# Optimization experiments

Measured on AMD Instinct MI355X. Metric: run time of the kernel, lower is better.

Reference implementation:

```python
import jax, jax.numpy as jnp
import numpy as np

N_QUBITS = 12
N_LAYERS = 3
DIM = 2 ** N_QUBITS


def _ry(t):
    # RY(t) = [[cos(t/2), -sin(t/2)], [sin(t/2), cos(t/2)]]; t scalar or (B,)
    c, s = jnp.cos(t / 2), jnp.sin(t / 2)
    return jnp.stack([jnp.stack([c, -s], -1), jnp.stack([s, c], -1)], -2).astype(jnp.complex64)


def _rx(t):
    c = jnp.cos(t / 2).astype(jnp.complex64)
    s = (-1j) * jnp.sin(t / 2).astype(jnp.complex64)
    return jnp.stack([jnp.stack([c, s], -1), jnp.stack([s, c], -1)], -2)


def _rz(t):
    e = jnp.exp(-0.5j * t.astype(jnp.complex64))
    z = jnp.zeros_like(e)
    return jnp.stack([jnp.stack([e, z], -1), jnp.stack([z, jnp.conj(e)], -1)], -2)


def _apply_1q(state, U, wire):
    # state: (B, 2^n); U: (2,2) shared or (B,2,2) per-sample
    B = state.shape[0]
    L, R = 2 ** wire, 2 ** (N_QUBITS - wire - 1)
    s = state.reshape(B, L, 2, R)
    sub = 'ab' if U.ndim == 2 else 'xab'
    s = jnp.einsum(f'{sub},xlbr->xlar', U, s)
    return s.reshape(B, DIM)


def _apply_cnot(state, ctrl):
    # CNOT on adjacent wires (ctrl, ctrl+1): flip target where control=1
    B = state.shape[0]
    L, R = 2 ** ctrl, 2 ** (N_QUBITS - ctrl - 2)
    s = state.reshape(B, L, 2, 2, R)
    s = jnp.concatenate([s[:, :, :1], s[:, :, 1:, ::-1]], axis=2)
    return s.reshape(B, DIM)


def _circuit(x, params):
    B = x.shape[0]
    state = jnp.zeros((B, DIM), jnp.complex64).at[:, 0].set(1.0)
    # input encoding: RY(x_i) on wire i (per-sample angles)
    for i in range(N_QUBITS):
        state = _apply_1q(state, _ry(x[:, i]), i)
    for layer in range(N_LAYERS):
        for q in range(N_QUBITS):
            state = _apply_1q(state, _ry(params[layer, q, 0]), q)
            state = _apply_1q(state, _rx(params[layer, q, 1]), q)
            state = _apply_1q(state, _rz(params[layer, q, 2]), q)
        for q in range(N_QUBITS - 1):
            state = _apply_cnot(state, q)
    probs = jnp.abs(state) ** 2  # wire 0 is the MSB, matching qml.probs
    p2 = probs[:, :2]
    return p2 / jnp.sum(p2, axis=1, keepdims=True)


def setup_inputs() -> dict:
    key = jax.random.key(0)
    k1, k2 = jax.random.split(key)
    x = (jax.random.uniform(k1, (8192, N_QUBITS), jnp.float32) * 2.0 - 1.0) * jnp.pi
    params = jax.random.normal(k2, (N_LAYERS, N_QUBITS, 3), jnp.float32) * 0.1
    return {"x": x, "params": params}


def reference(x, params):
    return _circuit(x, params)
```

## Files before the change

kernel.cpp:

```cpp
#include <hip/hip_runtime.h>
#include <math.h>

#define NQ  12
#define DIM 4096


__device__ float M_dev[DIM * 4];

struct Gate { float g00r, g00i, g01r, g01i; };

__device__ __forceinline__ Gate make_gate(const float* __restrict__ params,
                                          int layer, int q) {
  float p0 = params[(layer*NQ + q)*3 + 0];
  float p1 = params[(layer*NQ + q)*3 + 1];
  float p2 = params[(layer*NQ + q)*3 + 2];
  float s0, c0, s1, c1, sz, cz;
  __sincosf(0.5f*p0, &s0, &c0);
  __sincosf(0.5f*p1, &s1, &c1);
  __sincosf(0.5f*p2, &sz, &cz);
  float ur = c0*c1, ui = s0*s1, wr = s0*c1, wi = c0*s1;
  Gate g;
  g.g00r = cz*ur - sz*ui;  g.g00i = cz*ui + sz*ur;
  g.g01r = cz*wr + sz*wi;  g.g01i = cz*wi - sz*wr;
  return g;
}

__global__ __launch_bounds__(256) void qnn_prep(const float* __restrict__ params) {
  __shared__ float4 gtab[36];
  const int tid = threadIdx.x;
  if (tid < 36) {
    Gate g = make_gate(params, tid / 12, tid % 12);
    gtab[tid] = make_float4(g.g00r, g.g00i, g.g01r, g.g01i);
  }
  __syncthreads();

  const int blk = blockIdx.x;
  const int b   = blk >> 4;
  const int k   = ((blk & 15) << 8) | tid;

  float ur[4] = {1.f, 0.f, 0.f, 0.f};
  float ui[4] = {0.f, 0.f, 0.f, 0.f};

#pragma unroll
  for (int q = 0; q < 12; ++q) {
    float4 g1 = gtab[q];
    float4 g2 = gtab[12 + q];
    float4 g3 = gtab[24 + q];
    const int kq = (k >> (11 - q)) & 1;

    float arr = kq ? -g1.z : g1.x,  ari = kq ?  g1.w : g1.y;
    float brr = kq ?  g1.x : g1.z,  bri = kq ? -g1.y : g1.w;
    const int bq = (q == 11) ? b : 0;
    float A0r = bq ?  g3.z : g3.x,  A0i = bq ?  g3.w : g3.y;
    float A1r = bq ?  g3.x : -g3.z, A1i = bq ? -g3.y : g3.w;

    float tr[4], ti[4];
#pragma unroll
    for (int i = 0; i < 2; ++i) {
      float u0r = ur[i],     u0i = ui[i];
      float u1r = ur[2 + i], u1i = ui[2 + i];
      tr[i]     = u0r*arr - u0i*ari + u1r*brr - u1i*bri;
      ti[i]     = u0r*ari + u0i*arr + u1r*bri + u1i*brr;
      tr[2 + i] = u0r*brr - u0i*bri + u1r*arr - u1i*ari;
      ti[2 + i] = u0r*bri + u0i*brr + u1r*ari + u1i*arr;
    }
#pragma unroll
    for (int j = 0; j < 2; ++j) {
      float cjr = j ? -g2.z : g2.x, cji = j ?  g2.w : g2.y;
      float djr = j ?  g2.x : g2.z, dji = j ? -g2.y : g2.w;
      float t0r = tr[j*2], t0i = ti[j*2], t1r = tr[j*2+1], t1i = ti[j*2+1];
      float w0r = t0r*cjr - t0i*cji + t1r*djr - t1i*dji;
      float w0i = t0r*cji + t0i*cjr + t1r*dji + t1i*djr;
      float w1r = t0r*djr - t0i*dji + t1r*cjr - t1i*cji;
      float w1i = t0r*dji + t0i*djr + t1r*cji + t1i*cjr;
      ur[j*2]   = A0r*w0r - A0i*w0i;  ui[j*2]   = A0r*w0i + A0i*w0r;
      ur[j*2+1] = A1r*w1r - A1i*w1i;  ui[j*2+1] = A1r*w1i + A1i*w1r;
    }
  }

  float vr = (ur[0] + ur[1]) + (ur[2] + ur[3]);
  float vi = (ui[0] + ui[1]) + (ui[2] + ui[3]);
  ((float2*)M_dev)[2*k + b] = make_float2(vr, vi);
}


__global__ __launch_bounds__(256) void qnn_main(const float* __restrict__ x,
                                                float* __restrict__ out,
                                                int nbatch) {
  __shared__ float4 Ms[DIM];
  __shared__ float4 sLb[4 * 64];
  const float4* Mg = (const float4*)M_dev;
  for (int t = threadIdx.x; t < DIM; t += 256) Ms[t] = Mg[t];

  const int lane   = threadIdx.x & 63;
  const int wave   = threadIdx.x >> 6;
  const int batch0 = blockIdx.x * 16 + wave * 4;

  float sRv[4], sl[4];
#pragma unroll
  for (int b = 0; b < 4; ++b) {
    int bb = batch0 + b; if (bb >= nbatch) bb = nbatch - 1;
    const float* xb = x + (size_t)bb * NQ;
    float s, c, L = 1.f, R = 1.f;
#pragma unroll
    for (int w = 0; w < 6; ++w) {
      __sincosf(0.5f * xb[w], &s, &c);
      L *= ((lane >> (5 - w)) & 1) ? s : c;
    }
#pragma unroll
    for (int w = 6; w < 12; ++w) {
      __sincosf(0.5f * xb[w], &s, &c);
      R *= ((lane >> (11 - w)) & 1) ? s : c;
    }
    sl[b] = L; sRv[b] = R;
  }
  sLb[wave*64 + lane] = make_float4(sl[0], sl[1], sl[2], sl[3]);
  __syncthreads();

  float acc[4][4];
#pragma unroll
  for (int b = 0; b < 4; ++b)
#pragma unroll
    for (int c = 0; c < 4; ++c) acc[b][c] = 0.f;

#pragma unroll 4
  for (int i = 0; i < 64; ++i) {
    float4 m   = Ms[i * 64 + lane];
    float4 sv4 = sLb[wave*64 + i];
    float sv;
    sv = sv4.x * sRv[0];
    acc[0][0] = fmaf(m.x, sv, acc[0][0]); acc[0][1] = fmaf(m.y, sv, acc[0][1]);
    acc[0][2] = fmaf(m.z, sv, acc[0][2]); acc[0][3] = fmaf(m.w, sv, acc[0][3]);
    sv = sv4.y * sRv[1];
    acc[1][0] = fmaf(m.x, sv, acc[1][0]); acc[1][1] = fmaf(m.y, sv, acc[1][1]);
    acc[1][2] = fmaf(m.z, sv, acc[1][2]); acc[1][3] = fmaf(m.w, sv, acc[1][3]);
    sv = sv4.z * sRv[2];
    acc[2][0] = fmaf(m.x, sv, acc[2][0]); acc[2][1] = fmaf(m.y, sv, acc[2][1]);
    acc[2][2] = fmaf(m.z, sv, acc[2][2]); acc[2][3] = fmaf(m.w, sv, acc[2][3]);
    sv = sv4.w * sRv[3];
    acc[3][0] = fmaf(m.x, sv, acc[3][0]); acc[3][1] = fmaf(m.y, sv, acc[3][1]);
    acc[3][2] = fmaf(m.z, sv, acc[3][2]); acc[3][3] = fmaf(m.w, sv, acc[3][3]);
  }

#pragma unroll
  for (int off = 32; off > 0; off >>= 1)
#pragma unroll
    for (int b = 0; b < 4; ++b)
#pragma unroll
      for (int c = 0; c < 4; ++c)
        acc[b][c] += __shfl_xor(acc[b][c], off);

  if (lane == 0) {
#pragma unroll
    for (int b = 0; b < 4; ++b) {
      float p0 = acc[b][0]*acc[b][0] + acc[b][1]*acc[b][1];
      float p1 = acc[b][2]*acc[b][2] + acc[b][3]*acc[b][3];
      float inv = 1.0f / (p0 + p1);
      if (batch0 + b < nbatch)
        ((float2*)out)[batch0 + b] = make_float2(p0 * inv, p1 * inv);
    }
  }
}

extern "C" void kernel_launch(void* const* d_in, const int* in_sizes, int n_in,
                              void* d_out, int out_size, void* d_ws, size_t ws_size,
                              hipStream_t stream) {
  const float* x      = (const float*)d_in[0];
  const float* params = (const float*)d_in[1];
  float* out = (float*)d_out;
  (void)d_ws; (void)ws_size;

  const int nbatch = in_sizes[0] / NQ;
  qnn_prep<<<32, 256, 0, stream>>>(params);
  qnn_main<<<(nbatch + 15) / 16, 256, 0, stream>>>(x, out, nbatch);
}
```

Measured before the change: 70.32 us.

## Fuse into single per-sample kernel contracting product-state input through MPS-like chain

Replaces the two-kernel scheme, which built a 4096x4-entry transfer matrix and then ran a dense contraction per sample, with one kernel where each thread handles one sample. Because the encoded input is a product state, the thread folds the per-qubit cos/sin amplitudes directly into the 12-step gate chain with a 4-element complex carry. This removes the prep launch, the global matrix round trip and the 64-iteration dot product with shuffle reduction. The cost is 64-thread blocks, and the per-sample gate chain math is redone in every thread.

```diff
diff --git a/kernel.cpp b/kernel.cpp
--- a/kernel.cpp
+++ b/kernel.cpp
@@ -1,11 +1,8 @@
 #include <hip/hip_runtime.h>
 #include <math.h>
 
-#define NQ  12
-#define DIM 4096
+#define NQ 12
 
-
-__device__ float M_dev[DIM * 4];
 
 struct Gate { float g00r, g00i, g01r, g01i; };
 
@@ -25,7 +22,10 @@
   return g;
 }
 
-__global__ __launch_bounds__(256) void qnn_prep(const float* __restrict__ params) {
+__global__ __launch_bounds__(64) void qnn_fused(const float* __restrict__ x,
+                                                const float* __restrict__ params,
+                                                float* __restrict__ out,
+                                                int nbatch) {
   __shared__ float4 gtab[36];
   const int tid = threadIdx.x;
   if (tid < 36) {
@@ -34,25 +34,29 @@
   }
   __syncthreads();
 
-  const int blk = blockIdx.x;
-  const int b   = blk >> 4;
-  const int k   = ((blk & 15) << 8) | tid;
+  const int batch = blockIdx.x * 64 + tid;
+  int bb = batch < nbatch ? batch : nbatch - 1;
+
+  const float4* xv = (const float4*)(x + (size_t)bb * NQ);
+  float4 xa = xv[0], xm = xv[1], xz = xv[2];
+  float xs[12] = {xa.x, xa.y, xa.z, xa.w, xm.x, xm.y, xm.z, xm.w,
+                  xz.x, xz.y, xz.z, xz.w};
+  float cq[12], sq[12];
+#pragma unroll
+  for (int q = 0; q < 12; ++q) __sincosf(0.5f * xs[q], &sq[q], &cq[q]);
 
   float ur[4] = {1.f, 0.f, 0.f, 0.f};
   float ui[4] = {0.f, 0.f, 0.f, 0.f};
 
 #pragma unroll
-  for (int q = 0; q < 12; ++q) {
+  for (int q = 0; q < 11; ++q) {
     float4 g1 = gtab[q];
     float4 g2 = gtab[12 + q];
     float4 g3 = gtab[24 + q];
-    const int kq = (k >> (11 - q)) & 1;
+    const float c = cq[q], s = sq[q];
 
-    float arr = kq ? -g1.z : g1.x,  ari = kq ?  g1.w : g1.y;
-    float brr = kq ?  g1.x : g1.z,  bri = kq ? -g1.y : g1.w;
-    const int bq = (q == 11) ? b : 0;
-    float A0r = bq ?  g3.z : g3.x,  A0i = bq ?  g3.w : g3.y;
-    float A1r = bq ?  g3.x : -g3.z, A1i = bq ? -g3.y : g3.w;
+    float arr = c*g1.x - s*g1.z,  ari = c*g1.y + s*g1.w;
+    float brr = c*g1.z + s*g1.x,  bri = c*g1.w - s*g1.y;
 
     float tr[4], ti[4];
 #pragma unroll
@@ -64,6 +68,8 @@
       tr[2 + i] = u0r*brr - u0i*bri + u1r*arr - u1i*ari;
       ti[2 + i] = u0r*bri + u0i*brr + u1r*ari + u1i*arr;
     }
+    float A0r = g3.x, A0i = g3.y;
+    float A1r = -g3.z, A1i = g3.w;
 #pragma unroll
     for (int j = 0; j < 2; ++j) {
       float cjr = j ? -g2.z : g2.x, cji = j ?  g2.w : g2.y;
@@ -78,87 +84,42 @@
     }
   }
 
-  float vr = (ur[0] + ur[1]) + (ur[2] + ur[3]);
-  float vi = (ui[0] + ui[1]) + (ui[2] + ui[3]);
-  ((float2*)M_dev)[2*k + b] = make_float2(vr, vi);
-}
+  {
+    float4 g1 = gtab[11], g2 = gtab[23], g3 = gtab[35];
+    const float c = cq[11], s = sq[11];
+    float arr = c*g1.x - s*g1.z,  ari = c*g1.y + s*g1.w;
+    float brr = c*g1.z + s*g1.x,  bri = c*g1.w - s*g1.y;
+    float tr[4], ti[4];
+#pragma unroll
+    for (int i = 0; i < 2; ++i) {
+      float u0r = ur[i],     u0i = ui[i];
+      float u1r = ur[2 + i], u1i = ui[2 + i];
+      tr[i]     = u0r*arr - u0i*ari + u1r*brr - u1i*bri;
+      ti[i]     = u0r*ari + u0i*arr + u1r*bri + u1i*brr;
+      tr[2 + i] = u0r*brr - u0i*bri + u1r*arr - u1i*ari;
+      ti[2 + i] = u0r*bri + u0i*brr + u1r*ari + u1i*arr;
+    }
+    float W0r = 0.f, W0i = 0.f, W1r = 0.f, W1i = 0.f;
+#pragma unroll
+    for (int j = 0; j < 2; ++j) {
+      float cjr = j ? -g2.z : g2.x, cji = j ?  g2.w : g2.y;
+      float djr = j ?  g2.x : g2.z, dji = j ? -g2.y : g2.w;
+      float t0r = tr[j*2], t0i = ti[j*2], t1r = tr[j*2+1], t1i = ti[j*2+1];
+      W0r += t0r*cjr - t0i*cji + t1r*djr - t1i*dji;
+      W0i += t0r*cji + t0i*cjr + t1r*dji + t1i*djr;
+      W1r += t0r*djr - t0i*dji + t1r*cjr - t1i*cji;
+      W1i += t0r*dji + t0i*djr + t1r*cji + t1i*cjr;
+    }
+    float a0r = g3.x*W0r - g3.y*W0i - g3.z*W1r - g3.w*W1i;
+    float a0i = g3.x*W0i + g3.y*W0r - g3.z*W1i + g3.w*W1r;
+    float a1r = g3.z*W0r - g3.w*W0i + g3.x*W1r + g3.y*W1i;
+    float a1i = g3.z*W0i + g3.w*W0r + g3.x*W1i - g3.y*W1r;
 
-
-__global__ __launch_bounds__(256) void qnn_main(const float* __restrict__ x,
-                                                float* __restrict__ out,
-                                                int nbatch) {
-  __shared__ float4 Ms[DIM];
-  __shared__ float4 sLb[4 * 64];
-  const float4* Mg = (const float4*)M_dev;
-  for (int t = threadIdx.x; t < DIM; t += 256) Ms[t] = Mg[t];
-
-  const int lane   = threadIdx.x & 63;
-  const int wave   = threadIdx.x >> 6;
-  const int batch0 = blockIdx.x * 16 + wave * 4;
-
-  float sRv[4], sl[4];
-#pragma unroll
-  for (int b = 0; b < 4; ++b) {
-    int bb = batch0 + b; if (bb >= nbatch) bb = nbatch - 1;
-    const float* xb = x + (size_t)bb * NQ;
-    float s, c, L = 1.f, R = 1.f;
-#pragma unroll
-    for (int w = 0; w < 6; ++w) {
-      __sincosf(0.5f * xb[w], &s, &c);
-      L *= ((lane >> (5 - w)) & 1) ? s : c;
-    }
-#pragma unroll
-    for (int w = 6; w < 12; ++w) {
-      __sincosf(0.5f * xb[w], &s, &c);
-      R *= ((lane >> (11 - w)) & 1) ? s : c;
-    }
-    sl[b] = L; sRv[b] = R;
-  }
-  sLb[wave*64 + lane] = make_float4(sl[0], sl[1], sl[2], sl[3]);
-  __syncthreads();
-
-  float acc[4][4];
-#pragma unroll
-  for (int b = 0; b < 4; ++b)
-#pragma unroll
-    for (int c = 0; c < 4; ++c) acc[b][c] = 0.f;
-
-#pragma unroll 4
-  for (int i = 0; i < 64; ++i) {
-    float4 m   = Ms[i * 64 + lane];
-    float4 sv4 = sLb[wave*64 + i];
-    float sv;
-    sv = sv4.x * sRv[0];
-    acc[0][0] = fmaf(m.x, sv, acc[0][0]); acc[0][1] = fmaf(m.y, sv, acc[0][1]);
-    acc[0][2] = fmaf(m.z, sv, acc[0][2]); acc[0][3] = fmaf(m.w, sv, acc[0][3]);
-    sv = sv4.y * sRv[1];
-    acc[1][0] = fmaf(m.x, sv, acc[1][0]); acc[1][1] = fmaf(m.y, sv, acc[1][1]);
-    acc[1][2] = fmaf(m.z, sv, acc[1][2]); acc[1][3] = fmaf(m.w, sv, acc[1][3]);
-    sv = sv4.z * sRv[2];
-    acc[2][0] = fmaf(m.x, sv, acc[2][0]); acc[2][1] = fmaf(m.y, sv, acc[2][1]);
-    acc[2][2] = fmaf(m.z, sv, acc[2][2]); acc[2][3] = fmaf(m.w, sv, acc[2][3]);
-    sv = sv4.w * sRv[3];
-    acc[3][0] = fmaf(m.x, sv, acc[3][0]); acc[3][1] = fmaf(m.y, sv, acc[3][1]);
-    acc[3][2] = fmaf(m.z, sv, acc[3][2]); acc[3][3] = fmaf(m.w, sv, acc[3][3]);
-  }
-
-#pragma unroll
-  for (int off = 32; off > 0; off >>= 1)
-#pragma unroll
-    for (int b = 0; b < 4; ++b)
-#pragma unroll
-      for (int c = 0; c < 4; ++c)
-        acc[b][c] += __shfl_xor(acc[b][c], off);
-
-  if (lane == 0) {
-#pragma unroll
-    for (int b = 0; b < 4; ++b) {
-      float p0 = acc[b][0]*acc[b][0] + acc[b][1]*acc[b][1];
-      float p1 = acc[b][2]*acc[b][2] + acc[b][3]*acc[b][3];
-      float inv = 1.0f / (p0 + p1);
-      if (batch0 + b < nbatch)
-        ((float2*)out)[batch0 + b] = make_float2(p0 * inv, p1 * inv);
-    }
+    float p0 = a0r*a0r + a0i*a0i;
+    float p1 = a1r*a1r + a1i*a1i;
+    float inv = 1.0f / (p0 + p1);
+    if (batch < nbatch)
+      ((float2*)out)[batch] = make_float2(p0 * inv, p1 * inv);
   }
 }
 
@@ -171,6 +132,5 @@
   (void)d_ws; (void)ws_size;
 
   const int nbatch = in_sizes[0] / NQ;
-  qnn_prep<<<32, 256, 0, stream>>>(params);
-  qnn_main<<<(nbatch + 15) / 16, 256, 0, stream>>>(x, out, nbatch);
+  qnn_fused<<<(nbatch + 63) / 64, 64, 0, stream>>>(x, params, out, nbatch);
 }
```

Result: faster. 57.33 us (-18.5%).
